# Performance work log

Hardware: AMD Instinct MI355X
Metric: run time of the kernel (lower is better)

## Reference

```python
import jax, jax.numpy as jnp
import numpy as np
import math

D_MODEL = 1024
N_HEADS = 16
Q_PROJ = D_MODEL // 4
KV_PROJ = D_MODEL // 4
DH = D_MODEL // N_HEADS
LN_EPS = 1e-5


def _layernorm(x, gamma, beta):
    mu = jnp.mean(x, axis=-1, keepdims=True)
    var = jnp.mean(jnp.square(x - mu), axis=-1, keepdims=True)
    return (x - mu) * jax.lax.rsqrt(var + LN_EPS) * gamma + beta


def setup_inputs() -> dict:
    key = jax.random.key(0)
    ks = jax.random.split(key, 7)
    B, S = 2, 2048
    x = jax.random.normal(ks[0], (B, S, D_MODEL), dtype=jnp.float32)
    W_dq = 0.01 * jax.random.normal(ks[1], (D_MODEL, Q_PROJ), dtype=jnp.float32)
    W_uq = 0.01 * jax.random.normal(ks[2], (Q_PROJ, D_MODEL), dtype=jnp.float32)
    W_dkv = 0.01 * jax.random.normal(ks[3], (D_MODEL, KV_PROJ), dtype=jnp.float32)
    W_ukv = 0.01 * jax.random.normal(ks[4], (KV_PROJ, 2 * D_MODEL), dtype=jnp.float32)
    W_o = 0.01 * jax.random.normal(ks[5], (D_MODEL, D_MODEL), dtype=jnp.float32)
    return {
        "x": x,
        "W_dq": W_dq, "W_uq": W_uq,
        "q_ln_g": jnp.ones((Q_PROJ,), jnp.float32), "q_ln_b": jnp.zeros((Q_PROJ,), jnp.float32),
        "W_dkv": W_dkv, "W_ukv": W_ukv,
        "kv_ln_g": jnp.ones((KV_PROJ,), jnp.float32), "kv_ln_b": jnp.zeros((KV_PROJ,), jnp.float32),
        "W_o": W_o,
    }


def reference(x, W_dq, W_uq, q_ln_g, q_ln_b, W_dkv, W_ukv, kv_ln_g, kv_ln_b, W_o):
    B, S, D = x.shape
    # low-rank Q path
    cq = _layernorm(x @ W_dq, q_ln_g, q_ln_b)          # [B,S,q_proj]
    Q = cq @ W_uq                                       # [B,S,D]
    # low-rank KV path
    ckv = _layernorm(x @ W_dkv, kv_ln_g, kv_ln_b)       # [B,S,kv_proj]
    KV = ckv @ W_ukv                                    # [B,S,2D]
    K, V = KV[..., :D], KV[..., D:]
    q = Q.reshape(B, S, N_HEADS, DH)
    k = K.reshape(B, S, N_HEADS, DH)
    v = V.reshape(B, S, N_HEADS, DH)
    scores = jnp.einsum("bqhd,bkhd->bhqk", q, k) / math.sqrt(float(DH))
    # faithful to original: multiply by tril mask, then set exact zeros to -inf
    mask = jnp.tril(jnp.ones((S, S), dtype=scores.dtype))
    scores = scores * mask
    scores = jnp.where(scores == 0, -jnp.inf, scores)
    attn = jax.nn.softmax(scores, axis=-1)
    out = jnp.einsum("bhqk,bkhd->bqhd", attn, v).reshape(B, S, D)
    return out @ W_o.T
```

## Files before the change

kernel.cpp:

```cpp
#include <hip/hip_runtime.h>

typedef __bf16 bf16;
typedef __bf16 bf16x4 __attribute__((ext_vector_type(4)));
typedef __bf16 bf16x8 __attribute__((ext_vector_type(8)));
typedef float f32x4 __attribute__((ext_vector_type(4)));

#define D_MODEL 1024
#define PROJ    256
#define SEQ     2048
#define BATCH   2
#define TOK     4096
#define NH      16
#define DH      64
#define NEG_BIG (-1e30f)
#define QSCALE  0.18033688011112042f

#if __has_builtin(__builtin_amdgcn_exp2f)
#define EXP2(x) __builtin_amdgcn_exp2f(x)
#else
#define EXP2(x) exp2f(x)
#endif

typedef __attribute__((address_space(3))) unsigned int  lds_u32;
typedef __attribute__((address_space(1))) unsigned int  glb_u32;

__device__ __forceinline__ void gl2lds16(const void* gsrc, void* ldst) {
    __builtin_amdgcn_global_load_lds((const glb_u32*)gsrc, (lds_u32*)ldst, 16, 0, 0);
}

template <int CTRL>
__device__ __forceinline__ float dppmov(float x) {
    int i = __builtin_bit_cast(int, x);
    i = __builtin_amdgcn_update_dpp(i, i, CTRL, 0xf, 0xf, false);
    return __builtin_bit_cast(float, i);
}
__device__ __forceinline__ float rowsum16(float v) {
    v += dppmov<0xB1>(v);
    v += dppmov<0x4E>(v);
    v += dppmov<0x141>(v);
    v += dppmov<0x140>(v);
    return v;
}

__global__ void prep_weights_kernel(
    const float* __restrict__ W_o,  const float* __restrict__ W_dq,
    const float* __restrict__ W_dkv, const float* __restrict__ W_uq,
    const float* __restrict__ W_ukv, const float* __restrict__ x,
    bf16* __restrict__ Wo16, bf16* __restrict__ Wt_dq, bf16* __restrict__ Wt_dkv,
    bf16* __restrict__ Wt_uq, bf16* __restrict__ Wt_ukv, bf16* __restrict__ x16) {
    const int R0 = 1048576;
    const int R1 = R0 + 262144;
    const int R2 = R1 + 262144;
    const int R3 = R2 + 262144;
    const int R4 = R3 + 524288;
    const int R5 = R4 + 4194304;
    for (int i = blockIdx.x * blockDim.x + threadIdx.x; i < R5;
         i += gridDim.x * blockDim.x) {
        if (i < R0) {
            Wo16[i] = (bf16)W_o[i];
        } else if (i < R1) {
            int j = i - R0, n = j >> 10, k = j & 1023;
            Wt_dq[j] = (bf16)W_dq[k * 256 + n];
        } else if (i < R2) {
            int j = i - R1, n = j >> 10, k = j & 1023;
            Wt_dkv[j] = (bf16)W_dkv[k * 256 + n];
        } else if (i < R3) {
            int j = i - R2, n = j >> 8, k = j & 255;
            Wt_uq[j] = (bf16)W_uq[k * 1024 + n];
        } else if (i < R4) {
            int j = i - R3, n = j >> 8, k = j & 255;
            Wt_ukv[j] = (bf16)W_ukv[k * 2048 + n];
        } else {
            int j = i - R4;
            x16[j] = (bf16)x[j];
        }
    }
}

__global__ __launch_bounds__(256) void gemm_ln_kernel(
    const bf16* __restrict__ x16,
    const bf16* __restrict__ Wt_q, const bf16* __restrict__ Wt_kv,
    const float* __restrict__ q_g, const float* __restrict__ q_b,
    const float* __restrict__ kv_g, const float* __restrict__ kv_b,
    bf16* __restrict__ cq, bf16* __restrict__ ckv) {
    __shared__ alignas(16) bf16 xA[32 * 32];
    __shared__ alignas(16) bf16 wB[256 * 32];
    __shared__ float red1[4][16];
    __shared__ float red2[4][16];

    const int K = 1024;
    const bf16* Wt = blockIdx.y ? Wt_kv : Wt_q;
    const float* gamma = blockIdx.y ? kv_g : q_g;
    const float* beta  = blockIdx.y ? kv_b : q_b;
    bf16* out = blockIdx.y ? ckv : cq;

    const int m0 = blockIdx.x * 32;
    const int wv = threadIdx.x >> 6;
    const int lane = threadIdx.x & 63;
    const int g = lane >> 4;
    const int ln16 = lane & 15;
    const int wr = wv >> 1;
    const int wc = wv & 1;

    const int crow = lane >> 2;
    const int ckc = lane & 3;
    const bf16* gx = x16 + (size_t)(m0 + (wv & 1) * 16 + crow) * K + ckc * 8;
    char* lx = (char*)xA + (wv & 1) * 1024;
    const bf16* gw = Wt + (size_t)(64 * wv + crow) * K + ckc * 8;
    char* lw = (char*)wB + wv * 4096;

    f32x4 acc[8] = {};
    for (int k0 = 0; k0 < K; k0 += 32) {
        if (wv < 2) gl2lds16(gx + k0, lx);
#pragma unroll
        for (int i = 0; i < 4; ++i)
            gl2lds16(gw + (size_t)i * 16 * K + k0, lw + i * 1024);
        __syncthreads();

        bf16x8 a = *(const bf16x8*)(xA + (wr * 16 + ln16) * 32 + g * 8);
#pragma unroll
        for (int t = 0; t < 8; ++t) {
            bf16x8 b = *(const bf16x8*)(wB + (wc * 128 + 16 * t + ln16) * 32 + g * 8);
            acc[t] = __builtin_amdgcn_mfma_f32_16x16x32_bf16(a, b, acc[t], 0, 0, 0);
        }
        __syncthreads();
    }

    float s1[4], s2[4];
#pragma unroll
    for (int r = 0; r < 4; ++r) {
        float a = 0.f, b = 0.f;
#pragma unroll
        for (int t = 0; t < 8; ++t) { float v = acc[t][r]; a += v; b += v * v; }
        s1[r] = rowsum16(a); s2[r] = rowsum16(b);
    }
    if (ln16 == 0) {
#pragma unroll
        for (int r = 0; r < 4; ++r) {
            red1[wv][g * 4 + r] = s1[r];
            red2[wv][g * 4 + r] = s2[r];
        }
    }
    __syncthreads();
#pragma unroll
    for (int r = 0; r < 4; ++r) {
        int rl = g * 4 + r;
        float t1 = red1[wr * 2][rl] + red1[wr * 2 + 1][rl];
        float t2 = red2[wr * 2][rl] + red2[wr * 2 + 1][rl];
        float mu = t1 * (1.0f / 256.0f);
        float var = t2 * (1.0f / 256.0f) - mu * mu;
        float rs = rsqrtf(var + 1e-5f);
        int row = m0 + wr * 16 + rl;
#pragma unroll
        for (int t = 0; t < 8; ++t) {
            int col = wc * 128 + 16 * t + ln16;
            float v = (acc[t][r] - mu) * rs * gamma[col] + beta[col];
            out[(size_t)row * PROJ + col] = (bf16)v;
        }
    }
}

template <typename OutT>
__device__ __forceinline__ void gemm_body(
    const bf16* __restrict__ A, const bf16* __restrict__ Bt,
    OutT* __restrict__ C, bf16* __restrict__ C2, int N, int K,
    int bx, int by, int mode, bf16* tA, bf16* tB) {
    const int w = threadIdx.x >> 6;
    const int lane = threadIdx.x & 63;
    const int g = lane >> 4;
    const int ln16 = lane & 15;
    const int wr = w >> 1;
    const int wc = w & 1;

    const int m0 = bx * 64;
    const int n0 = by * 128;

    const int crow = lane >> 2;
    const int ckc = lane & 3;
    const bf16* gA  = A  + (size_t)(m0 + w * 16 + crow) * K + ckc * 8;
    const bf16* gB0 = Bt + (size_t)(n0 + w * 16 + crow) * K + ckc * 8;
    const bf16* gB1 = Bt + (size_t)(n0 + 64 + w * 16 + crow) * K + ckc * 8;
    char* lA  = (char*)tA + w * 1024;
    char* lB0 = (char*)tB + w * 1024;
    char* lB1 = (char*)tB + 4096 + w * 1024;

    f32x4 acc[2][4] = {};
    for (int k0 = 0; k0 < K; k0 += 32) {
        gl2lds16(gA + k0, lA);
        gl2lds16(gB0 + k0, lB0);
        gl2lds16(gB1 + k0, lB1);
        __syncthreads();

        bf16x8 af[2], bf[4];
#pragma unroll
        for (int s = 0; s < 2; ++s)
            af[s] = *(const bf16x8*)(tA + (wr * 32 + s * 16 + ln16) * 32 + g * 8);
#pragma unroll
        for (int t = 0; t < 4; ++t)
            bf[t] = *(const bf16x8*)(tB + (wc * 64 + t * 16 + ln16) * 32 + g * 8);
#pragma unroll
        for (int s = 0; s < 2; ++s)
#pragma unroll
            for (int t = 0; t < 4; ++t)
                acc[s][t] = __builtin_amdgcn_mfma_f32_16x16x32_bf16(
                    af[s], bf[t], acc[s][t], 0, 0, 0);
        __syncthreads();
    }

#pragma unroll
    for (int s = 0; s < 2; ++s)
#pragma unroll
        for (int t = 0; t < 4; ++t) {
            const int col = n0 + wc * 64 + t * 16 + ln16;
            const int tok0 = m0 + wr * 32 + s * 16 + g * 4;
            if (mode == 2 && col >= 1024) {
                int cc = col - 1024;
                int h = cc >> 6, d = cc & 63;
                int b = tok0 >> 11, sq = tok0 & 2047;
                bf16x4 pk;
#pragma unroll
                for (int r = 0; r < 4; ++r) pk[r] = (bf16)acc[s][t][r];
                *(bf16x4*)(C2 + ((size_t)((b * 16 + h) * 64 + d) * SEQ + sq)) = pk;
            } else {
#pragma unroll
                for (int r = 0; r < 4; ++r) {
                    int row = tok0 + r;
                    float v = acc[s][t][r];
                    if (mode == 0) {
                        C[(size_t)row * N + col] = (OutT)v;
                    } else {
                        if (mode == 1) v *= QSCALE;
                        int h = col >> 6, d = col & 63;
                        int b = row >> 11, sq = row & 2047;
                        C[((size_t)((b * 16 + h) * 2048 + sq)) * 64 + d] = (OutT)v;
                    }
                }
            }
        }
}

__global__ __launch_bounds__(256) void gemm_o_kernel(
    const bf16* __restrict__ A, const bf16* __restrict__ Bt,
    float* __restrict__ C, int M, int N, int K) {
    __shared__ alignas(16) bf16 tA[64 * 32];
    __shared__ alignas(16) bf16 tB[128 * 32];
    gemm_body<float>(A, Bt, C, nullptr, N, K, blockIdx.x, blockIdx.y, 0, tA, tB);
}

__global__ __launch_bounds__(256) void gemm_qkv_kernel(
    const bf16* __restrict__ cq, const bf16* __restrict__ Wt_uq,
    const bf16* __restrict__ ckv, const bf16* __restrict__ Wt_ukv,
    bf16* __restrict__ Qh, bf16* __restrict__ Kh, bf16* __restrict__ Vt) {
    __shared__ alignas(16) bf16 tA[64 * 32];
    __shared__ alignas(16) bf16 tB[128 * 32];
    const int i = blockIdx.x;
    if (i < 512) {
        gemm_body<bf16>(cq, Wt_uq, Qh, nullptr, D_MODEL, PROJ,
                        i >> 3, i & 7, 1, tA, tB);
    } else {
        const int j = i - 512;
        gemm_body<bf16>(ckv, Wt_ukv, Kh, Vt, 2 * D_MODEL, PROJ,
                        j >> 4, j & 15, 2, tA, tB);
    }
}

__device__ __forceinline__ void qk_exp_pack(
    int k0, int q, bool masked, int g, int ln16,
    bf16x8 aq0, bf16x8 aq1, const bf16x8* Kf,
    float& li, bf16x8& P1, bf16x8& P2) {
    f32x4 sc[4];
#pragma unroll
    for (int c = 0; c < 4; ++c) {
        f32x4 z = {};
        z = __builtin_amdgcn_mfma_f32_16x16x32_bf16(Kf[2 * c], aq0, z, 0, 0, 0);
        z = __builtin_amdgcn_mfma_f32_16x16x32_bf16(Kf[2 * c + 1], aq1, z, 0, 0, 0);
        sc[c] = z;
    }
    if (masked) {
        const int kb = k0 + 8 * g;
#pragma unroll
        for (int c = 0; c < 4; ++c)
#pragma unroll
            for (int r = 0; r < 4; ++r) {
                int kcol = kb + (c & 1) * 4 + r + ((c >> 1) << 5);
                if (kcol > q) sc[c][r] = NEG_BIG;
            }
    }
#pragma unroll
    for (int c = 0; c < 4; ++c)
#pragma unroll
        for (int r = 0; r < 4; ++r) {
            float p = EXP2(sc[c][r]);
            sc[c][r] = p;
            li += p;
        }
#pragma unroll
    for (int r = 0; r < 4; ++r) {
        P1[r] = (bf16)sc[0][r]; P1[4 + r] = (bf16)sc[1][r];
        P2[r] = (bf16)sc[2][r]; P2[4 + r] = (bf16)sc[3][r];
    }
}

__device__ __forceinline__ void pv_accum(
    bf16x8 P1, bf16x8 P2, const bf16x8* Vf, f32x4* o) {
#pragma unroll
    for (int t = 0; t < 4; ++t) {
        o[t] = __builtin_amdgcn_mfma_f32_16x16x32_bf16(Vf[2 * t], P1, o[t], 0, 0, 0);
        o[t] = __builtin_amdgcn_mfma_f32_16x16x32_bf16(Vf[2 * t + 1], P2, o[t], 0, 0, 0);
    }
}

__global__ __launch_bounds__(128) void attn_kernel(
    const bf16* __restrict__ Qh, const bf16* __restrict__ Kh,
    const bf16* __restrict__ Vt, bf16* __restrict__ AT) {
    __shared__ alignas(128) bf16 kbuf[2][64 * 64];
    __shared__ alignas(128) bf16 vbuf[2][64 * 64];

    const int lane = threadIdx.x & 63;
    const int g = lane >> 4;
    const int ln16 = lane & 15;
    const int wv = threadIdx.x >> 6;

    const int bh = blockIdx.x & 31;
    const int pr = blockIdx.x >> 5;

    const bf16* Kbh = Kh + (size_t)bh * SEQ * DH;
    const bf16* Vbh = Vt + (size_t)bh * DH * SEQ;

    const int rho = lane >> 3;
    const int sl  = lane & 7;
    int kofs[4];
    size_t vofs[4];
#pragma unroll
    for (int i = 0; i < 4; ++i) {
        const int row = 32 * wv + 8 * i + rho;
        const int c = sl ^ ((rho & 3) | ((i & 1) << 2));
        kofs[i] = row * 64 + c * 8;
        vofs[i] = (size_t)row * SEQ + c * 8;
    }

    const int row_base = ((ln16 & 12) << 1) + (ln16 & 3);
    int kro[4], vro[4];
#pragma unroll
    for (int c = 0; c < 4; ++c) {
        const int row = row_base + (c & 1) * 4 + ((c >> 1) << 5);
        const int fr = (row & 3) | (((row >> 3) & 1) << 2);
        kro[c] = row * 128 + (g ^ fr) * 16;
    }
#pragma unroll
    for (int t = 0; t < 4; ++t) {
        const int d = 16 * t + ln16;
        const int fd = (d & 3) | (((d >> 3) & 1) << 2);
        vro[t] = d * 128 + (g ^ fd) * 16;
    }

    const int b = bh >> 4, h = bh & 15;

    for (int ph = 0; ph < 2; ++ph) {
        const int super = ph ? pr : 31 - pr;
        const int nt = super + 1;
        const int qb = super * 64 + wv * 32;

        bf16x8 aq[2][2];
#pragma unroll
        for (int hh = 0; hh < 2; ++hh) {
            const bf16* qp =
                Qh + ((size_t)bh * SEQ + qb + 16 * hh + ln16) * DH + g * 8;
            aq[hh][0] = *(const bf16x8*)qp;
            aq[hh][1] = *(const bf16x8*)(qp + 32);
        }

        f32x4 o0[4] = {}, o1[4] = {};
        float li0 = 0.f, li1 = 0.f;

#pragma unroll
        for (int i = 0; i < 4; ++i) {
            gl2lds16(Kbh + kofs[i], (char*)kbuf + wv * 4096 + i * 1024);
            gl2lds16(Vbh + vofs[i], (char*)vbuf + wv * 4096 + i * 1024);
        }
        __syncthreads();

        int cur = 0;
        for (int kt = 0; kt < nt; ++kt) {
            if (kt + 1 < nt) {
                const size_t k0n = (size_t)(kt + 1) * 64;
                char* kb = (char*)kbuf + (cur ^ 1) * 8192 + wv * 4096;
                char* vb = (char*)vbuf + (cur ^ 1) * 8192 + wv * 4096;
#pragma unroll
                for (int i = 0; i < 4; ++i) {
                    gl2lds16(Kbh + k0n * 64 + kofs[i], kb + i * 1024);
                    gl2lds16(Vbh + vofs[i] + k0n, vb + i * 1024);
                }
            }

            const char* kb = (const char*)kbuf + cur * 8192;
            const char* vb = (const char*)vbuf + cur * 8192;
            bf16x8 Kf[8], Vf[8];
#pragma unroll
            for (int c = 0; c < 4; ++c) {
                Kf[2 * c]     = *(const bf16x8*)(kb + kro[c]);
                Kf[2 * c + 1] = *(const bf16x8*)(kb + (kro[c] ^ 64));
            }
#pragma unroll
            for (int t = 0; t < 4; ++t) {
                Vf[2 * t]     = *(const bf16x8*)(vb + vro[t]);
                Vf[2 * t + 1] = *(const bf16x8*)(vb + (vro[t] ^ 64));
            }

            const int k0 = kt * 64;
            const bool msk = (kt == super);
            bf16x8 P1a, P2a, P1b, P2b;
            qk_exp_pack(k0, qb + ln16, msk, g, ln16,
                        aq[0][0], aq[0][1], Kf, li0, P1a, P2a);
            qk_exp_pack(k0, qb + 16 + ln16, msk, g, ln16,
                        aq[1][0], aq[1][1], Kf, li1, P1b, P2b);
            pv_accum(P1a, P2a, Vf, o0);
            pv_accum(P1b, P2b, Vf, o1);
            __syncthreads();
            cur ^= 1;
        }

        li0 += __shfl_xor(li0, 16); li0 += __shfl_xor(li0, 32);
        li1 += __shfl_xor(li1, 16); li1 += __shfl_xor(li1, 32);
        const float inv0 = 1.0f / li0, inv1 = 1.0f / li1;
        const size_t tok0 = (size_t)(b * SEQ + qb + ln16) * D_MODEL + h * DH;
        const size_t tok1 = (size_t)(b * SEQ + qb + 16 + ln16) * D_MODEL + h * DH;
#pragma unroll
        for (int t = 0; t < 4; ++t) {
            bf16x4 pk0, pk1;
#pragma unroll
            for (int r = 0; r < 4; ++r) {
                pk0[r] = (bf16)(o0[t][r] * inv0);
                pk1[r] = (bf16)(o1[t][r] * inv1);
            }
            *(bf16x4*)(AT + tok0 + 16 * t + 4 * g) = pk0;
            *(bf16x4*)(AT + tok1 + 16 * t + 4 * g) = pk1;
        }
    }
}

extern "C" void kernel_launch(void* const* d_in, const int* in_sizes, int n_in,
                              void* d_out, int out_size, void* d_ws, size_t ws_size,
                              hipStream_t stream) {
    const float* x     = (const float*)d_in[0];
    const float* W_dq  = (const float*)d_in[1];
    const float* W_uq  = (const float*)d_in[2];
    const float* q_g   = (const float*)d_in[3];
    const float* q_b   = (const float*)d_in[4];
    const float* W_dkv = (const float*)d_in[5];
    const float* W_ukv = (const float*)d_in[6];
    const float* kv_g  = (const float*)d_in[7];
    const float* kv_b  = (const float*)d_in[8];
    const float* W_o   = (const float*)d_in[9];

    char* ws = (char*)d_ws;
    size_t off = 0;
    bf16* Wo16   = (bf16*)(ws + off); off += (size_t)D_MODEL * D_MODEL * 2;
    bf16* Wt_dq  = (bf16*)(ws + off); off += (size_t)PROJ * D_MODEL * 2;
    bf16* Wt_dkv = (bf16*)(ws + off); off += (size_t)PROJ * D_MODEL * 2;
    bf16* Wt_uq  = (bf16*)(ws + off); off += (size_t)D_MODEL * PROJ * 2;
    bf16* Wt_ukv = (bf16*)(ws + off); off += (size_t)(2 * D_MODEL) * PROJ * 2;
    bf16* x16    = (bf16*)(ws + off); off += (size_t)TOK * D_MODEL * 2;
    bf16* cq     = (bf16*)(ws + off); off += (size_t)TOK * PROJ * 2;
    bf16* ckv    = (bf16*)(ws + off); off += (size_t)TOK * PROJ * 2;
    bf16* Qh     = (bf16*)(ws + off); off += (size_t)TOK * D_MODEL * 2;
    bf16* Kh     = (bf16*)(ws + off); off += (size_t)TOK * D_MODEL * 2;
    bf16* Vt     = (bf16*)(ws + off); off += (size_t)TOK * D_MODEL * 2;
    bf16* AT     = (bf16*)(ws + off); off += (size_t)TOK * D_MODEL * 2;

    prep_weights_kernel<<<2048, 256, 0, stream>>>(
        W_o, W_dq, W_dkv, W_uq, W_ukv, x,
        Wo16, Wt_dq, Wt_dkv, Wt_uq, Wt_ukv, x16);

    gemm_ln_kernel<<<dim3(TOK / 32, 2), 256, 0, stream>>>(
        x16, Wt_dq, Wt_dkv, q_g, q_b, kv_g, kv_b, cq, ckv);

    gemm_qkv_kernel<<<1536, 256, 0, stream>>>(cq, Wt_uq, ckv, Wt_ukv, Qh, Kh, Vt);

    attn_kernel<<<512, 128, 0, stream>>>(Qh, Kh, Vt, AT);

    gemm_o_kernel<<<dim3(TOK / 64, D_MODEL / 128), 256, 0, stream>>>(
        AT, Wo16, (float*)d_out, TOK, D_MODEL, D_MODEL);
}
```

Baseline: 205.5 us.

## Use 4-wave 128-query attention blocks with MFMA row-sum and setprio

Restructures the attention kernel so each 256-thread block handles a 128-query super-tile with four waves sharing each K/V tile in LDS, replacing the two-phase per-block loop with one tile per block balanced across two rounds. Each wave loads half as many rows per tile, and waves whose queries lie before a key tile skip compute but still join the barrier. The softmax denominator is now computed by an extra MFMA against a ones vector instead of scalar adds plus cross-lane shuffles. MFMA sections are wrapped in s_setprio to favour matrix issue. Risks include idle waves on diagonal tiles and extra MFMA work for the row sum.

```diff
diff --git a/kernel.cpp b/kernel.cpp
--- a/kernel.cpp
+++ b/kernel.cpp
@@ -267,8 +267,9 @@
 __device__ __forceinline__ void qk_exp_pack(
     int k0, int q, bool masked, int g, int ln16,
     bf16x8 aq0, bf16x8 aq1, const bf16x8* Kf,
-    float& li, bf16x8& P1, bf16x8& P2) {
+    bf16x8& P1, bf16x8& P2) {
     f32x4 sc[4];
+    __builtin_amdgcn_s_setprio(1);
 #pragma unroll
     for (int c = 0; c < 4; ++c) {
         f32x4 z = {};
@@ -276,6 +277,7 @@
         z = __builtin_amdgcn_mfma_f32_16x16x32_bf16(Kf[2 * c + 1], aq1, z, 0, 0, 0);
         sc[c] = z;
     }
+    __builtin_amdgcn_s_setprio(0);
     if (masked) {
         const int kb = k0 + 8 * g;
 #pragma unroll
@@ -289,11 +291,7 @@
 #pragma unroll
     for (int c = 0; c < 4; ++c)
 #pragma unroll
-        for (int r = 0; r < 4; ++r) {
-            float p = EXP2(sc[c][r]);
-            sc[c][r] = p;
-            li += p;
-        }
+        for (int r = 0; r < 4; ++r) sc[c][r] = EXP2(sc[c][r]);
 #pragma unroll
     for (int r = 0; r < 4; ++r) {
         P1[r] = (bf16)sc[0][r]; P1[4 + r] = (bf16)sc[1][r];
@@ -302,15 +300,20 @@
 }
 
 __device__ __forceinline__ void pv_accum(
-    bf16x8 P1, bf16x8 P2, const bf16x8* Vf, f32x4* o) {
+    bf16x8 P1, bf16x8 P2, const bf16x8* Vf, bf16x8 vones,
+    f32x4* o, f32x4& oli) {
+    __builtin_amdgcn_s_setprio(1);
 #pragma unroll
     for (int t = 0; t < 4; ++t) {
         o[t] = __builtin_amdgcn_mfma_f32_16x16x32_bf16(Vf[2 * t], P1, o[t], 0, 0, 0);
         o[t] = __builtin_amdgcn_mfma_f32_16x16x32_bf16(Vf[2 * t + 1], P2, o[t], 0, 0, 0);
     }
-}
-
-__global__ __launch_bounds__(128) void attn_kernel(
+    oli = __builtin_amdgcn_mfma_f32_16x16x32_bf16(vones, P1, oli, 0, 0, 0);
+    oli = __builtin_amdgcn_mfma_f32_16x16x32_bf16(vones, P2, oli, 0, 0, 0);
+    __builtin_amdgcn_s_setprio(0);
+}
+
+__global__ __launch_bounds__(256) void attn_kernel(
     const bf16* __restrict__ Qh, const bf16* __restrict__ Kh,
     const bf16* __restrict__ Vt, bf16* __restrict__ AT) {
     __shared__ alignas(128) bf16 kbuf[2][64 * 64];
@@ -321,19 +324,24 @@
     const int ln16 = lane & 15;
     const int wv = threadIdx.x >> 6;
 
-    const int bh = blockIdx.x & 31;
-    const int pr = blockIdx.x >> 5;
+    const int j = blockIdx.x & 255;
+    const int rnd = blockIdx.x >> 8;
+    const int bh = j & 31;
+    const int gg = j >> 5;
+    const int super = rnd ? gg : 15 - gg;
+    const int nt = 2 * super + 2;
+    const int qb = super * 128 + wv * 32;
 
     const bf16* Kbh = Kh + (size_t)bh * SEQ * DH;
     const bf16* Vbh = Vt + (size_t)bh * DH * SEQ;
 
     const int rho = lane >> 3;
     const int sl  = lane & 7;
-    int kofs[4];
-    size_t vofs[4];
-#pragma unroll
-    for (int i = 0; i < 4; ++i) {
-        const int row = 32 * wv + 8 * i + rho;
+    int kofs[2];
+    size_t vofs[2];
+#pragma unroll
+    for (int i = 0; i < 2; ++i) {
+        const int row = 16 * wv + 8 * i + rho;
         const int c = sl ^ ((rho & 3) | ((i & 1) << 2));
         kofs[i] = row * 64 + c * 8;
         vofs[i] = (size_t)row * SEQ + c * 8;
@@ -354,45 +362,42 @@
         vro[t] = d * 128 + (g ^ fd) * 16;
     }
 
-    const int b = bh >> 4, h = bh & 15;
-
-    for (int ph = 0; ph < 2; ++ph) {
-        const int super = ph ? pr : 31 - pr;
-        const int nt = super + 1;
-        const int qb = super * 64 + wv * 32;
-
-        bf16x8 aq[2][2];
-#pragma unroll
-        for (int hh = 0; hh < 2; ++hh) {
-            const bf16* qp =
-                Qh + ((size_t)bh * SEQ + qb + 16 * hh + ln16) * DH + g * 8;
-            aq[hh][0] = *(const bf16x8*)qp;
-            aq[hh][1] = *(const bf16x8*)(qp + 32);
-        }
-
-        f32x4 o0[4] = {}, o1[4] = {};
-        float li0 = 0.f, li1 = 0.f;
-
-#pragma unroll
-        for (int i = 0; i < 4; ++i) {
-            gl2lds16(Kbh + kofs[i], (char*)kbuf + wv * 4096 + i * 1024);
-            gl2lds16(Vbh + vofs[i], (char*)vbuf + wv * 4096 + i * 1024);
-        }
-        __syncthreads();
-
-        int cur = 0;
-        for (int kt = 0; kt < nt; ++kt) {
-            if (kt + 1 < nt) {
-                const size_t k0n = (size_t)(kt + 1) * 64;
-                char* kb = (char*)kbuf + (cur ^ 1) * 8192 + wv * 4096;
-                char* vb = (char*)vbuf + (cur ^ 1) * 8192 + wv * 4096;
-#pragma unroll
-                for (int i = 0; i < 4; ++i) {
-                    gl2lds16(Kbh + k0n * 64 + kofs[i], kb + i * 1024);
-                    gl2lds16(Vbh + vofs[i] + k0n, vb + i * 1024);
-                }
+    bf16x8 aq[2][2];
+#pragma unroll
+    for (int hh = 0; hh < 2; ++hh) {
+        const bf16* qp = Qh + ((size_t)bh * SEQ + qb + 16 * hh + ln16) * DH + g * 8;
+        aq[hh][0] = *(const bf16x8*)qp;
+        aq[hh][1] = *(const bf16x8*)(qp + 32);
+    }
+
+    bf16x8 vones;
+#pragma unroll
+    for (int i = 0; i < 8; ++i) vones[i] = (bf16)1.0f;
+
+    f32x4 o0[4] = {}, o1[4] = {};
+    f32x4 oli0 = {}, oli1 = {};
+
+#pragma unroll
+    for (int i = 0; i < 2; ++i) {
+        gl2lds16(Kbh + kofs[i], (char*)kbuf + wv * 2048 + i * 1024);
+        gl2lds16(Vbh + vofs[i], (char*)vbuf + wv * 2048 + i * 1024);
+    }
+    __syncthreads();
+
+    int cur = 0;
+    for (int kt = 0; kt < nt; ++kt) {
+        if (kt + 1 < nt) {
+            const size_t k0n = (size_t)(kt + 1) * 64;
+            char* kb = (char*)kbuf + (cur ^ 1) * 8192 + wv * 2048;
+            char* vb = (char*)vbuf + (cur ^ 1) * 8192 + wv * 2048;
+#pragma unroll
+            for (int i = 0; i < 2; ++i) {
+                gl2lds16(Kbh + k0n * 64 + kofs[i], kb + i * 1024);
+                gl2lds16(Vbh + vofs[i] + k0n, vb + i * 1024);
             }
-
+        }
+
+        if (kt * 64 <= qb + 31) {
             const char* kb = (const char*)kbuf + cur * 8192;
             const char* vb = (const char*)vbuf + cur * 8192;
             bf16x8 Kf[8], Vf[8];
@@ -408,34 +413,34 @@
             }
 
             const int k0 = kt * 64;
-            const bool msk = (kt == super);
+            const bool msk = (64 * (kt + 1) > qb);
             bf16x8 P1a, P2a, P1b, P2b;
             qk_exp_pack(k0, qb + ln16, msk, g, ln16,
-                        aq[0][0], aq[0][1], Kf, li0, P1a, P2a);
+                        aq[0][0], aq[0][1], Kf, P1a, P2a);
             qk_exp_pack(k0, qb + 16 + ln16, msk, g, ln16,
-                        aq[1][0], aq[1][1], Kf, li1, P1b, P2b);
-            pv_accum(P1a, P2a, Vf, o0);
-            pv_accum(P1b, P2b, Vf, o1);
-            __syncthreads();
-            cur ^= 1;
-        }
-
-        li0 += __shfl_xor(li0, 16); li0 += __shfl_xor(li0, 32);
-        li1 += __shfl_xor(li1, 16); li1 += __shfl_xor(li1, 32);
-        const float inv0 = 1.0f / li0, inv1 = 1.0f / li1;
-        const size_t tok0 = (size_t)(b * SEQ + qb + ln16) * D_MODEL + h * DH;
-        const size_t tok1 = (size_t)(b * SEQ + qb + 16 + ln16) * D_MODEL + h * DH;
-#pragma unroll
-        for (int t = 0; t < 4; ++t) {
-            bf16x4 pk0, pk1;
-#pragma unroll
-            for (int r = 0; r < 4; ++r) {
-                pk0[r] = (bf16)(o0[t][r] * inv0);
-                pk1[r] = (bf16)(o1[t][r] * inv1);
-            }
-            *(bf16x4*)(AT + tok0 + 16 * t + 4 * g) = pk0;
-            *(bf16x4*)(AT + tok1 + 16 * t + 4 * g) = pk1;
-        }
+                        aq[1][0], aq[1][1], Kf, P1b, P2b);
+            pv_accum(P1a, P2a, Vf, vones, o0, oli0);
+            pv_accum(P1b, P2b, Vf, vones, o1, oli1);
+        }
+        __syncthreads();
+        cur ^= 1;
+    }
+
+    const float inv0 = 1.0f / oli0[0];
+    const float inv1 = 1.0f / oli1[0];
+    const int b = bh >> 4, h = bh & 15;
+    const size_t tok0 = (size_t)(b * SEQ + qb + ln16) * D_MODEL + h * DH;
+    const size_t tok1 = (size_t)(b * SEQ + qb + 16 + ln16) * D_MODEL + h * DH;
+#pragma unroll
+    for (int t = 0; t < 4; ++t) {
+        bf16x4 pk0, pk1;
+#pragma unroll
+        for (int r = 0; r < 4; ++r) {
+            pk0[r] = (bf16)(o0[t][r] * inv0);
+            pk1[r] = (bf16)(o1[t][r] * inv1);
+        }
+        *(bf16x4*)(AT + tok0 + 16 * t + 4 * g) = pk0;
+        *(bf16x4*)(AT + tok1 + 16 * t + 4 * g) = pk1;
     }
 }
 
@@ -477,7 +482,7 @@
 
     gemm_qkv_kernel<<<1536, 256, 0, stream>>>(cq, Wt_uq, ckv, Wt_ukv, Qh, Kh, Vt);
 
-    attn_kernel<<<512, 128, 0, stream>>>(Qh, Kh, Vt, AT);
+    attn_kernel<<<512, 256, 0, stream>>>(Qh, Kh, Vt, AT);
 
     gemm_o_kernel<<<dim3(TOK / 64, D_MODEL / 128), 256, 0, stream>>>(
         AT, Wo16, (float*)d_out, TOK, D_MODEL, D_MODEL);
```

Result: no change. 203.4 us (-1.0%).
